# Kernel tuning notes

Hardware: AMD Instinct MI355X
Metric: run time of the kernel (lower is better)

The kernel has to match this reference:

```python
import jax, jax.numpy as jnp
import numpy as np

B, S, D_MODEL, H = 4, 2048, 1024, 16
DEPTH = D_MODEL // H  # 64


def setup_inputs() -> dict:
    key = jax.random.key(0)
    ks = jax.random.split(key, 12)
    inp = {
        "v": jax.random.normal(ks[0], (B, S, D_MODEL), jnp.float32),
        "k": jax.random.normal(ks[1], (B, S, D_MODEL), jnp.float32),
        "q": jax.random.normal(ks[2], (B, S, D_MODEL), jnp.float32),
        "mask": jnp.zeros((B, 1, 1, S), jnp.int32),  # unused by the layer
        # Dense(d_model) params (glorot-ish scale)
        "wq": jax.random.normal(ks[3], (D_MODEL, D_MODEL), jnp.float32) / np.sqrt(D_MODEL),
        "bq": jnp.zeros((D_MODEL,), jnp.float32),
        "wk": jax.random.normal(ks[4], (D_MODEL, D_MODEL), jnp.float32) / np.sqrt(D_MODEL),
        "bk": jnp.zeros((D_MODEL,), jnp.float32),
        "wv": jax.random.normal(ks[5], (D_MODEL, D_MODEL), jnp.float32) / np.sqrt(D_MODEL),
        "bv": jnp.zeros((D_MODEL,), jnp.float32),
        # global attention weights: [max_seq_len, 1], stddev=0.1
        "gqw": 0.1 * jax.random.normal(ks[6], (S, 1), jnp.float32),
        "gkw": 0.1 * jax.random.normal(ks[7], (S, 1), jnp.float32),
        "wo": jax.random.normal(ks[8], (D_MODEL, D_MODEL), jnp.float32) / np.sqrt(D_MODEL),
        "bo": jnp.zeros((D_MODEL,), jnp.float32),
    }
    return inp


def _split_heads(x):
    # [B, S, D] -> [B, H, S, depth]
    Bc = x.shape[0]
    return x.reshape(Bc, -1, H, DEPTH).transpose(0, 2, 1, 3)


def reference(v, k, q, mask, wq, bq, wk, bk, wv, bv, gqw, gkw, wo, bo):
    # QKV projections
    qh = _split_heads(q @ wq + bq)  # [B, H, S, depth]
    kh = _split_heads(k @ wk + bk)
    vh = _split_heads(v @ wv + bv)
    # Fastformer additive attention: mul -> seq-sum -> mul -> seq-sum -> mul -> add
    qh = qh * gqw                          # gqw [S,1] broadcasts over [B,H,S,depth]
    gq = jnp.sum(qh, axis=2, keepdims=True)  # global query [B,H,1,depth]
    kh = kh * gq * gkw
    gk = jnp.sum(kh, axis=2, keepdims=True)  # global key [B,H,1,depth]
    out = vh * gk + qh                       # [B,H,S,depth]
    # merge heads and output projection
    out = out.transpose(0, 2, 1, 3).reshape(out.shape[0], -1, D_MODEL)
    return out @ wo + bo
```

## Files before the change

### kernel.cpp

```cpp
#include <hip/hip_runtime.h>

#define DM 1024
#define BATCH 4
#define SEQ 2048
#define M_TOT (BATCH*SEQ)

typedef unsigned short ushort_t;
typedef __bf16 bf16x8 __attribute__((ext_vector_type(8)));
typedef float f32x4 __attribute__((ext_vector_type(4)));
typedef unsigned short u16x4 __attribute__((ext_vector_type(4)));
typedef unsigned short u16x8 __attribute__((ext_vector_type(8)));

__device__ __forceinline__ ushort_t f2bf(float f) {
  unsigned u = __builtin_bit_cast(unsigned, f);
  u = (u + 0x7fffu + ((u >> 16) & 1u)) >> 16;
  return (ushort_t)u;
}
__device__ __forceinline__ float bf2f(ushort_t h) {
  unsigned u = ((unsigned)h) << 16;
  return __builtin_bit_cast(float, u);
}

#define GLL(gp, lp)                                                            \
  __builtin_amdgcn_global_load_lds(                                            \
      (const __attribute__((address_space(1))) unsigned int*)(const void*)(gp),\
      (__attribute__((address_space(3))) unsigned int*)(void*)(lp), 16, 0, 0)

__global__ void k_reduce(const float* __restrict__ q, const float* __restrict__ k,
                         const float* __restrict__ v,
                         const float* __restrict__ gqw, const float* __restrict__ gkw,
                         float* __restrict__ pq, float* __restrict__ pk,
                         float* __restrict__ G,
                         ushort_t* __restrict__ qb, ushort_t* __restrict__ vb) {
  const int b = blockIdx.x, sc = blockIdx.y;
  const int d0 = threadIdx.x * 4;
  const int s0 = sc * 16;
  const size_t base = ((size_t)b * SEQ + s0) * DM + d0;
  float aq0 = 0.f, aq1 = 0.f, aq2 = 0.f, aq3 = 0.f;
  float ak0 = 0.f, ak1 = 0.f, ak2 = 0.f, ak3 = 0.f;
  float sgq = 0.f, sgk = 0.f;
#pragma unroll 4
  for (int i = 0; i < 16; ++i) {
    const float wq_ = gqw[s0 + i], wk_ = gkw[s0 + i];
    const size_t off = base + (size_t)i * DM;
    const float4 qv = *(const float4*)(q + off);
    const float4 kv = *(const float4*)(k + off);
    const float4 vv = *(const float4*)(v + off);
    aq0 += wq_ * qv.x; aq1 += wq_ * qv.y; aq2 += wq_ * qv.z; aq3 += wq_ * qv.w;
    ak0 += wk_ * kv.x; ak1 += wk_ * kv.y; ak2 += wk_ * kv.z; ak3 += wk_ * kv.w;
    u16x4 oq, ov;
    oq[0] = f2bf(wq_ * qv.x); oq[1] = f2bf(wq_ * qv.y);
    oq[2] = f2bf(wq_ * qv.z); oq[3] = f2bf(wq_ * qv.w);
    ov[0] = f2bf(vv.x); ov[1] = f2bf(vv.y); ov[2] = f2bf(vv.z); ov[3] = f2bf(vv.w);
    *(u16x4*)(qb + off) = oq;
    *(u16x4*)(vb + off) = ov;
    sgq += wq_; sgk += wk_;
  }
  const size_t po = ((size_t)(sc * BATCH + b) << 10) + d0;
  *(float4*)(pq + po) = make_float4(aq0, aq1, aq2, aq3);
  *(float4*)(pk + po) = make_float4(ak0, ak1, ak2, ak3);
  if (b == 0 && threadIdx.x == 0) {
    atomicAdd(&G[0], sgq);
    atomicAdd(&G[1], sgk);
  }
}

__global__ void k_gpart(const float* __restrict__ wq, const float* __restrict__ wk,
                        const float* __restrict__ pq, const float* __restrict__ pk,
                        float* __restrict__ qacc, float* __restrict__ kacc) {
  const int d = blockIdx.x * 256 + threadIdx.x;
  const int k0 = blockIdx.y * 32;
  __shared__ float sq[4][32], sk[4][32];
  if (threadIdx.x < 128) {
    const int b = threadIdx.x >> 5, kk = threadIdx.x & 31;
    float aq = 0.f, ak = 0.f;
#pragma unroll 4
    for (int s = 0; s < 128; ++s) {
      const size_t po = ((size_t)(s * BATCH + b) << 10) + k0 + kk;
      aq += pq[po];
      ak += pk[po];
    }
    sq[b][kk] = aq;
    sk[b][kk] = ak;
  }
  __syncthreads();
  float aq[4] = {0.f, 0.f, 0.f, 0.f}, ak[4] = {0.f, 0.f, 0.f, 0.f};
#pragma unroll 8
  for (int kk = 0; kk < 32; ++kk) {
    const float wqv = wq[(size_t)(k0 + kk) * DM + d];
    const float wkv = wk[(size_t)(k0 + kk) * DM + d];
#pragma unroll
    for (int b = 0; b < 4; ++b) {
      aq[b] += sq[b][kk] * wqv;
      ak[b] += sk[b][kk] * wkv;
    }
  }
#pragma unroll
  for (int b = 0; b < 4; ++b) {
    atomicAdd(&qacc[b * DM + d], aq[b]);
    atomicAdd(&kacc[b * DM + d], ak[b]);
  }
}

__global__ void k_wprep(const float* __restrict__ wq, const float* __restrict__ wv,
                        const float* __restrict__ wo,
                        ushort_t* __restrict__ wqB, ushort_t* __restrict__ wvB,
                        ushort_t* __restrict__ woT) {
  const int bid = blockIdx.x;
  if (bid < 1024) {
    const float* x = bid < 512 ? wq : wv;
    ushort_t* y = bid < 512 ? wqB : wvB;
    size_t i = (size_t)(bid & 511) * 256 + threadIdx.x;
    const float4* p = (const float4*)x + i * 2;
    float4 a = p[0], bb = p[1];
    u16x8 o;
    o[0] = f2bf(a.x); o[1] = f2bf(a.y); o[2] = f2bf(a.z); o[3] = f2bf(a.w);
    o[4] = f2bf(bb.x); o[5] = f2bf(bb.y); o[6] = f2bf(bb.z); o[7] = f2bf(bb.w);
    *(u16x8*)(y + i * 8) = o;
  } else {
    __shared__ float ls[32][33];
    const int t = bid - 1024;
    const int bi = t >> 5, bj = t & 31;
#pragma unroll
    for (int p = 0; p < 4; ++p) {
      int e = threadIdx.x + p * 256;
      int r = e >> 5, c = e & 31;
      ls[r][c] = wo[(size_t)(bi * 32 + r) * DM + bj * 32 + c];
    }
    __syncthreads();
#pragma unroll
    for (int p = 0; p < 4; ++p) {
      int e = threadIdx.x + p * 256;
      int r = e >> 5, c = e & 31;
      woT[(size_t)(bj * 32 + r) * DM + bi * 32 + c] = f2bf(ls[c][r]);
    }
  }
}

__global__ void k_wogbias(const ushort_t* __restrict__ woT, const float* __restrict__ wo,
                          const float* __restrict__ qacc, const float* __restrict__ kacc,
                          const float* __restrict__ bq, const float* __restrict__ bk,
                          const float* __restrict__ bv, const float* __restrict__ G,
                          ushort_t* __restrict__ wogT,
                          float* __restrict__ qbias, float* __restrict__ vbias) {
  const int bid = blockIdx.x;
  const float G0 = G[0], G1 = G[1];
  if (bid < 2048) {
    const size_t i = (size_t)bid * 256 + threadIdx.x;
    const size_t c = i * 8;
    const int j0 = (int)(c & (DM - 1));
    const int b = (int)(c >> 20);
    u16x8 wv8 = *(const u16x8*)(woT + (c & ((1u << 20) - 1)));
    const float4 qa0 = *(const float4*)(qacc + b * DM + j0);
    const float4 qa1 = *(const float4*)(qacc + b * DM + j0 + 4);
    const float4 ka0 = *(const float4*)(kacc + b * DM + j0);
    const float4 ka1 = *(const float4*)(kacc + b * DM + j0 + 4);
    const float4 bq0 = *(const float4*)(bq + j0);
    const float4 bq1 = *(const float4*)(bq + j0 + 4);
    const float4 bk0 = *(const float4*)(bk + j0);
    const float4 bk1 = *(const float4*)(bk + j0 + 4);
    float qa[8] = {qa0.x, qa0.y, qa0.z, qa0.w, qa1.x, qa1.y, qa1.z, qa1.w};
    float ka[8] = {ka0.x, ka0.y, ka0.z, ka0.w, ka1.x, ka1.y, ka1.z, ka1.w};
    float bqv[8] = {bq0.x, bq0.y, bq0.z, bq0.w, bq1.x, bq1.y, bq1.z, bq1.w};
    float bkv[8] = {bk0.x, bk0.y, bk0.z, bk0.w, bk1.x, bk1.y, bk1.z, bk1.w};
    u16x8 o;
#pragma unroll
    for (int j = 0; j < 8; ++j) {
      const float gk = (qa[j] + bqv[j] * G0) * (ka[j] + bkv[j] * G1);
      o[j] = f2bf(bf2f(wv8[j]) * gk);
    }
    *(u16x8*)(wogT + i * 8) = o;
  } else {
    const int t = bid - 2048;
    const int n = (t & 3) * 256 + threadIdx.x;
    const int k0 = (t >> 2) * 32;
    float aq = 0.f, av[4] = {0.f, 0.f, 0.f, 0.f};
    for (int kk = 0; kk < 32; ++kk) {
      const int j = k0 + kk;
      const float w = wo[(size_t)j * DM + n];
      aq += bq[j] * w;
      const float bw = bv[j] * w;
      const float bqj = bq[j] * G0, bkj = bk[j] * G1;
#pragma unroll
      for (int b = 0; b < 4; ++b) {
        const float gkv = (qacc[b * DM + j] + bqj) * (kacc[b * DM + j] + bkj);
        av[b] += bw * gkv;
      }
    }
    atomicAdd(&qbias[n], aq);
#pragma unroll
    for (int b = 0; b < 4; ++b) atomicAdd(&vbias[b * DM + n], av[b]);
  }
}

template <int MODE, int NT>
__global__ __launch_bounds__(512, 1)
void k_pipe(const ushort_t* __restrict__ A0, const ushort_t* __restrict__ B0,
            const ushort_t* __restrict__ A1, const ushort_t* __restrict__ B1,
            const float* __restrict__ gqw, const float* __restrict__ qbias,
            const float* __restrict__ vbias, const float* __restrict__ bo,
            void* __restrict__ OutV) {
  __shared__ __align__(16) ushort_t lsA[3][256 * 64];
  __shared__ __align__(16) ushort_t lsB[3][128 * 64];
  const int tid = threadIdx.x;
  const int w = tid >> 6, lane = tid & 63;
  const int m0 = blockIdx.x * 256, n0 = blockIdx.y * 128;
  const int b = (MODE == 0) ? (m0 >> 11) : 0;
  const int wr = w >> 1, wc = w & 1;

  const ushort_t *Aq, *Bq, *Av = nullptr, *Bv = nullptr;
  if constexpr (MODE == 0) {
    Aq = A0; Bq = B0; Av = A1; Bv = B1 + (size_t)b * (DM * DM);
  } else {
    const int z = blockIdx.z;
    Aq = z ? A1 + (size_t)(z - 1) * (DM * DM) : A0;
    Bq = z ? B1 : B0;
  }

  const int subrow = lane >> 3;
  const int srcslot = (lane & 7) ^ subrow;
  size_t offA[4], offB[2];
#pragma unroll
  for (int p = 0; p < 4; ++p) {
    const int row = (4 * w + p) * 8 + subrow;
    offA[p] = (size_t)(m0 + row) * DM + srcslot * 8;
  }
#pragma unroll
  for (int p = 0; p < 2; ++p) {
    const int row = (2 * w + p) * 8 + subrow;
    offB[p] = (size_t)(n0 + row) * DM + srcslot * 8;
  }

  const int g = lane >> 4, l7 = lane & 7, l15 = lane & 15;
  int aoff[2][4], boff[2][4];
#pragma unroll
  for (int kh = 0; kh < 2; ++kh) {
#pragma unroll
    for (int i = 0; i < 4; ++i) {
      const int ra = wr * 64 + i * 16 + l15;
      aoff[kh][i] = ra * 64 + (((kh * 4 + g) ^ l7) * 8);
    }
#pragma unroll
    for (int j = 0; j < 4; ++j) {
      const int rb = wc * 64 + j * 16 + l15;
      boff[kh][j] = rb * 64 + (((kh * 4 + g) ^ l7) * 8);
    }
  }

  f32x4 acc[4][4];
#pragma unroll
  for (int i = 0; i < 4; ++i)
#pragma unroll
    for (int j = 0; j < 4; ++j) acc[i][j] = (f32x4){0.f, 0.f, 0.f, 0.f};

  auto SRC = [&](int tt, const ushort_t*& Ab, const ushort_t*& Bb, int& k0) {
    if (MODE == 0 && tt >= NT / 2) { Ab = Av; Bb = Bv; k0 = (tt - NT / 2) * 64; }
    else                           { Ab = Aq; Bb = Bq; k0 = tt * 64; }
  };
  auto STAGE_H0 = [&](int tt, int buf) {
    const ushort_t *Ab, *Bb; int k0; SRC(tt, Ab, Bb, k0);
    GLL(Ab + offA[0] + k0, &lsA[buf][(4 * w + 0) * 512]);
    GLL(Ab + offA[1] + k0, &lsA[buf][(4 * w + 1) * 512]);
    GLL(Bb + offB[0] + k0, &lsB[buf][(2 * w + 0) * 512]);
  };
  auto STAGE_H1 = [&](int tt, int buf) {
    const ushort_t *Ab, *Bb; int k0; SRC(tt, Ab, Bb, k0);
    GLL(Ab + offA[2] + k0, &lsA[buf][(4 * w + 2) * 512]);
    GLL(Ab + offA[3] + k0, &lsA[buf][(4 * w + 3) * 512]);
    GLL(Bb + offB[1] + k0, &lsB[buf][(2 * w + 1) * 512]);
  };
  auto READF = [&](bf16x8 (&av)[4], bf16x8 (&bv)[4], int cur, int kh) {
#pragma unroll
    for (int i = 0; i < 4; ++i) av[i] = *(const bf16x8*)(&lsA[cur][aoff[kh][i]]);
#pragma unroll
    for (int j = 0; j < 4; ++j) bv[j] = *(const bf16x8*)(&lsB[cur][boff[kh][j]]);
  };
  auto DOMFMA = [&](bf16x8 (&av)[4], bf16x8 (&bv)[4]) {
    __builtin_amdgcn_s_setprio(1);
#pragma unroll
    for (int i = 0; i < 4; ++i)
#pragma unroll
      for (int j = 0; j < 4; ++j)
        acc[i][j] = __builtin_amdgcn_mfma_f32_16x16x32_bf16(av[i], bv[j], acc[i][j], 0, 0, 0);
    __builtin_amdgcn_s_setprio(0);
  };

  bf16x8 avA[4], bvA[4], avB[4], bvB[4];

  STAGE_H0(0, 0); STAGE_H1(0, 0);
  STAGE_H0(1, 1); STAGE_H1(1, 1);
  asm volatile("s_waitcnt vmcnt(6)" ::: "memory");
  __builtin_amdgcn_s_barrier();
  READF(avA, bvA, 0, 0);

#pragma unroll 1
  for (int t = 0; t < NT; ++t) {
    const int cur = t % 3, nb = (t + 2) % 3, nxt = (t + 1) % 3;
    READF(avB, bvB, cur, 1);
    if (t + 2 < NT) STAGE_H0(t + 2, nb);
    DOMFMA(avA, bvA);
    if (t + 1 < NT) {
      if (t + 2 < NT) { asm volatile("s_waitcnt vmcnt(3)\n\ts_barrier" ::: "memory"); }
      else            { asm volatile("s_waitcnt vmcnt(0)\n\ts_barrier" ::: "memory"); }
      READF(avA, bvA, nxt, 0);
      if (t + 2 < NT) STAGE_H1(t + 2, nb);
    }
    DOMFMA(avB, bvB);
  }

  const int lr = (lane >> 4) * 4, lc = lane & 15;
  const int rbase = m0 + wr * 64, cbase = n0 + wc * 64;
  if constexpr (MODE == 0) {
    float* Out = (float*)OutV;
#pragma unroll
    for (int j = 0; j < 4; ++j) {
      const int col = cbase + j * 16 + lc;
      const float qbn = qbias[col];
      const float cb = vbias[b * DM + col] + bo[col];
#pragma unroll
      for (int i = 0; i < 4; ++i)
#pragma unroll
        for (int r = 0; r < 4; ++r) {
          const int row = rbase + i * 16 + lr + r;
          Out[(size_t)row * DM + col] = acc[i][j][r] + gqw[row & (SEQ - 1)] * qbn + cb;
        }
    }
  } else {
    ushort_t* Out = (ushort_t*)OutV + (size_t)blockIdx.z * (DM * DM);
#pragma unroll
    for (int j = 0; j < 4; ++j) {
      const int col = cbase + j * 16 + lc;
#pragma unroll
      for (int i = 0; i < 4; ++i)
#pragma unroll
        for (int r = 0; r < 4; ++r) {
          const int row = rbase + i * 16 + lr + r;
          Out[(size_t)row * DM + col] = f2bf(acc[i][j][r]);
        }
    }
  }
}

extern "C" void kernel_launch(void* const* d_in, const int* in_sizes, int n_in,
                              void* d_out, int out_size, void* d_ws, size_t ws_size,
                              hipStream_t stream) {
  const float* v   = (const float*)d_in[0];
  const float* k   = (const float*)d_in[1];
  const float* q   = (const float*)d_in[2];
  const float* wq  = (const float*)d_in[4];
  const float* bq  = (const float*)d_in[5];
  const float* wk  = (const float*)d_in[6];
  const float* bk  = (const float*)d_in[7];
  const float* wv  = (const float*)d_in[8];
  const float* bv  = (const float*)d_in[9];
  const float* gqw = (const float*)d_in[10];
  const float* gkw = (const float*)d_in[11];
  const float* wo  = (const float*)d_in[12];
  const float* bo  = (const float*)d_in[13];
  float* out = (float*)d_out;
  float* wsf = (float*)d_ws;

  float* qacc  = wsf + 8192;
  float* kacc  = wsf + 12288;
  float* G     = wsf + 16384;
  float* qbias = wsf + 16640;
  float* vbias = wsf + 17664;
  ushort_t* b16  = (ushort_t*)((char*)d_ws + (1 << 17));
  ushort_t* qb   = b16;
  ushort_t* vb   = qb + (size_t)M_TOT * DM;
  ushort_t* wqB  = vb + (size_t)M_TOT * DM;
  ushort_t* wvB  = wqB + (size_t)DM * DM;
  ushort_t* woT  = wvB + (size_t)DM * DM;
  ushort_t* WqoT = woT + (size_t)DM * DM;
  ushort_t* WvbT = WqoT + (size_t)DM * DM;
  ushort_t* wogT = (ushort_t*)out;
  float* pq = out + (1 << 22);
  float* pk = pq + (1 << 20);

  hipMemsetAsync((char*)d_ws + 8192 * sizeof(float), 0,
                 (21760 - 8192) * sizeof(float), stream);

  k_wprep<<<2048, 256, 0, stream>>>(wq, wv, wo, wqB, wvB, woT);

  k_reduce<<<dim3(BATCH, SEQ / 16), 256, 0, stream>>>(q, k, v, gqw, gkw, pq, pk, G, qb, vb);

  k_gpart<<<dim3(DM / 256, DM / 32), 256, 0, stream>>>(wq, wk, pq, pk, qacc, kacc);

  k_wogbias<<<2176, 256, 0, stream>>>(woT, wo, qacc, kacc, bq, bk, bv, G,
                                      wogT, qbias, vbias);

  k_pipe<1, 16><<<dim3(4, 8, 5), 512, 0, stream>>>(
      woT, wqB, wogT, wvB, nullptr, nullptr, nullptr, nullptr, WqoT);

  k_pipe<0, 32><<<dim3(M_TOT / 256, DM / 128), 512, 0, stream>>>(
      qb, WqoT, vb, WvbT, gqw, qbias, vbias, bo, out);
}
```

Measured before the change: 124.8 us.

## Fuse weight prep into reduce kernel and split partial-sum reduction out of gpart

```diff
diff --git a/kernel.cpp b/kernel.cpp
--- a/kernel.cpp
+++ b/kernel.cpp
@@ -26,91 +26,53 @@
       (const __attribute__((address_space(1))) unsigned int*)(const void*)(gp),\
       (__attribute__((address_space(3))) unsigned int*)(void*)(lp), 16, 0, 0)
 
-__global__ void k_reduce(const float* __restrict__ q, const float* __restrict__ k,
-                         const float* __restrict__ v,
-                         const float* __restrict__ gqw, const float* __restrict__ gkw,
-                         float* __restrict__ pq, float* __restrict__ pk,
-                         float* __restrict__ G,
-                         ushort_t* __restrict__ qb, ushort_t* __restrict__ vb) {
-  const int b = blockIdx.x, sc = blockIdx.y;
-  const int d0 = threadIdx.x * 4;
-  const int s0 = sc * 16;
-  const size_t base = ((size_t)b * SEQ + s0) * DM + d0;
-  float aq0 = 0.f, aq1 = 0.f, aq2 = 0.f, aq3 = 0.f;
-  float ak0 = 0.f, ak1 = 0.f, ak2 = 0.f, ak3 = 0.f;
-  float sgq = 0.f, sgk = 0.f;
+__global__ void k_prep_reduce(const float* __restrict__ q, const float* __restrict__ k,
+                              const float* __restrict__ v,
+                              const float* __restrict__ gqw, const float* __restrict__ gkw,
+                              const float* __restrict__ wq, const float* __restrict__ wv,
+                              const float* __restrict__ wo,
+                              float* __restrict__ pq, float* __restrict__ pk,
+                              float* __restrict__ G,
+                              ushort_t* __restrict__ qb, ushort_t* __restrict__ vb,
+                              ushort_t* __restrict__ wqB, ushort_t* __restrict__ wvB,
+                              ushort_t* __restrict__ woT) {
+  const int bid = blockIdx.x;
+  if (bid < 512) {
+    const int b = bid & 3, sc = bid >> 2;
+    const int d0 = threadIdx.x * 4;
+    const int s0 = sc * 16;
+    const size_t base = ((size_t)b * SEQ + s0) * DM + d0;
+    float aq0 = 0.f, aq1 = 0.f, aq2 = 0.f, aq3 = 0.f;
+    float ak0 = 0.f, ak1 = 0.f, ak2 = 0.f, ak3 = 0.f;
+    float sgq = 0.f, sgk = 0.f;
 #pragma unroll 4
-  for (int i = 0; i < 16; ++i) {
-    const float wq_ = gqw[s0 + i], wk_ = gkw[s0 + i];
-    const size_t off = base + (size_t)i * DM;
-    const float4 qv = *(const float4*)(q + off);
-    const float4 kv = *(const float4*)(k + off);
-    const float4 vv = *(const float4*)(v + off);
-    aq0 += wq_ * qv.x; aq1 += wq_ * qv.y; aq2 += wq_ * qv.z; aq3 += wq_ * qv.w;
-    ak0 += wk_ * kv.x; ak1 += wk_ * kv.y; ak2 += wk_ * kv.z; ak3 += wk_ * kv.w;
-    u16x4 oq, ov;
-    oq[0] = f2bf(wq_ * qv.x); oq[1] = f2bf(wq_ * qv.y);
-    oq[2] = f2bf(wq_ * qv.z); oq[3] = f2bf(wq_ * qv.w);
-    ov[0] = f2bf(vv.x); ov[1] = f2bf(vv.y); ov[2] = f2bf(vv.z); ov[3] = f2bf(vv.w);
-    *(u16x4*)(qb + off) = oq;
-    *(u16x4*)(vb + off) = ov;
-    sgq += wq_; sgk += wk_;
-  }
-  const size_t po = ((size_t)(sc * BATCH + b) << 10) + d0;
-  *(float4*)(pq + po) = make_float4(aq0, aq1, aq2, aq3);
-  *(float4*)(pk + po) = make_float4(ak0, ak1, ak2, ak3);
-  if (b == 0 && threadIdx.x == 0) {
-    atomicAdd(&G[0], sgq);
-    atomicAdd(&G[1], sgk);
-  }
-}
-
-__global__ void k_gpart(const float* __restrict__ wq, const float* __restrict__ wk,
-                        const float* __restrict__ pq, const float* __restrict__ pk,
-                        float* __restrict__ qacc, float* __restrict__ kacc) {
-  const int d = blockIdx.x * 256 + threadIdx.x;
-  const int k0 = blockIdx.y * 32;
-  __shared__ float sq[4][32], sk[4][32];
-  if (threadIdx.x < 128) {
-    const int b = threadIdx.x >> 5, kk = threadIdx.x & 31;
-    float aq = 0.f, ak = 0.f;
-#pragma unroll 4
-    for (int s = 0; s < 128; ++s) {
-      const size_t po = ((size_t)(s * BATCH + b) << 10) + k0 + kk;
-      aq += pq[po];
-      ak += pk[po];
-    }
-    sq[b][kk] = aq;
-    sk[b][kk] = ak;
-  }
-  __syncthreads();
-  float aq[4] = {0.f, 0.f, 0.f, 0.f}, ak[4] = {0.f, 0.f, 0.f, 0.f};
-#pragma unroll 8
-  for (int kk = 0; kk < 32; ++kk) {
-    const float wqv = wq[(size_t)(k0 + kk) * DM + d];
-    const float wkv = wk[(size_t)(k0 + kk) * DM + d];
-#pragma unroll
-    for (int b = 0; b < 4; ++b) {
-      aq[b] += sq[b][kk] * wqv;
-      ak[b] += sk[b][kk] * wkv;
-    }
-  }
-#pragma unroll
-  for (int b = 0; b < 4; ++b) {
-    atomicAdd(&qacc[b * DM + d], aq[b]);
-    atomicAdd(&kacc[b * DM + d], ak[b]);
-  }
-}
-
-__global__ void k_wprep(const float* __restrict__ wq, const float* __restrict__ wv,
-                        const float* __restrict__ wo,
-                        ushort_t* __restrict__ wqB, ushort_t* __restrict__ wvB,
-                        ushort_t* __restrict__ woT) {
-  const int bid = blockIdx.x;
-  if (bid < 1024) {
-    const float* x = bid < 512 ? wq : wv;
-    ushort_t* y = bid < 512 ? wqB : wvB;
-    size_t i = (size_t)(bid & 511) * 256 + threadIdx.x;
+    for (int i = 0; i < 16; ++i) {
+      const float wq_ = gqw[s0 + i], wk_ = gkw[s0 + i];
+      const size_t off = base + (size_t)i * DM;
+      const float4 qv = *(const float4*)(q + off);
+      const float4 kv = *(const float4*)(k + off);
+      const float4 vv = *(const float4*)(v + off);
+      aq0 += wq_ * qv.x; aq1 += wq_ * qv.y; aq2 += wq_ * qv.z; aq3 += wq_ * qv.w;
+      ak0 += wk_ * kv.x; ak1 += wk_ * kv.y; ak2 += wk_ * kv.z; ak3 += wk_ * kv.w;
+      u16x4 oq, ov;
+      oq[0] = f2bf(wq_ * qv.x); oq[1] = f2bf(wq_ * qv.y);
+      oq[2] = f2bf(wq_ * qv.z); oq[3] = f2bf(wq_ * qv.w);
+      ov[0] = f2bf(vv.x); ov[1] = f2bf(vv.y); ov[2] = f2bf(vv.z); ov[3] = f2bf(vv.w);
+      *(u16x4*)(qb + off) = oq;
+      *(u16x4*)(vb + off) = ov;
+      sgq += wq_; sgk += wk_;
+    }
+    const size_t po = ((size_t)(sc * BATCH + b) << 10) + d0;
+    *(float4*)(pq + po) = make_float4(aq0, aq1, aq2, aq3);
+    *(float4*)(pk + po) = make_float4(ak0, ak1, ak2, ak3);
+    if (b == 0 && threadIdx.x == 0) {
+      atomicAdd(&G[0], sgq);
+      atomicAdd(&G[1], sgk);
+    }
+  } else if (bid < 1536) {
+    const float* x = bid < 1024 ? wq : wv;
+    ushort_t* y = bid < 1024 ? wqB : wvB;
+    size_t i = (size_t)((bid - 512) & 511) * 256 + threadIdx.x;
     const float4* p = (const float4*)x + i * 2;
     float4 a = p[0], bb = p[1];
     u16x8 o;
@@ -119,7 +81,7 @@
     *(u16x8*)(y + i * 8) = o;
   } else {
     __shared__ float ls[32][33];
-    const int t = bid - 1024;
+    const int t = bid - 1536;
     const int bi = t >> 5, bj = t & 31;
 #pragma unroll
     for (int p = 0; p < 4; ++p) {
@@ -134,6 +96,52 @@
       int r = e >> 5, c = e & 31;
       woT[(size_t)(bj * 32 + r) * DM + bi * 32 + c] = f2bf(ls[c][r]);
     }
+  }
+}
+
+__global__ void k_rsum(const float* __restrict__ pq, const float* __restrict__ pk,
+                       float* __restrict__ qr, float* __restrict__ kr) {
+  const int b = blockIdx.x;
+  const int d = blockIdx.y * 256 + threadIdx.x;
+  const int sg = blockIdx.z;
+  float aq = 0.f, ak = 0.f;
+#pragma unroll 4
+  for (int s = sg * 32; s < sg * 32 + 32; ++s) {
+    const size_t po = ((size_t)(s * BATCH + b) << 10) + d;
+    aq += pq[po];
+    ak += pk[po];
+  }
+  atomicAdd(&qr[b * DM + d], aq);
+  atomicAdd(&kr[b * DM + d], ak);
+}
+
+__global__ void k_gpart(const float* __restrict__ wq, const float* __restrict__ wk,
+                        const float* __restrict__ qr, const float* __restrict__ kr,
+                        float* __restrict__ qacc, float* __restrict__ kacc) {
+  const int d = blockIdx.x * 256 + threadIdx.x;
+  const int k0 = blockIdx.y * 32;
+  __shared__ float sq[4][32], sk[4][32];
+  if (threadIdx.x < 128) {
+    const int b = threadIdx.x >> 5, kk = threadIdx.x & 31;
+    sq[b][kk] = qr[b * DM + k0 + kk];
+    sk[b][kk] = kr[b * DM + k0 + kk];
+  }
+  __syncthreads();
+  float aq[4] = {0.f, 0.f, 0.f, 0.f}, ak[4] = {0.f, 0.f, 0.f, 0.f};
+#pragma unroll 8
+  for (int kk = 0; kk < 32; ++kk) {
+    const float wqv = wq[(size_t)(k0 + kk) * DM + d];
+    const float wkv = wk[(size_t)(k0 + kk) * DM + d];
+#pragma unroll
+    for (int b = 0; b < 4; ++b) {
+      aq[b] += sq[b][kk] * wqv;
+      ak[b] += sk[b][kk] * wkv;
+    }
+  }
+#pragma unroll
+  for (int b = 0; b < 4; ++b) {
+    atomicAdd(&qacc[b * DM + d], aq[b]);
+    atomicAdd(&kacc[b * DM + d], ak[b]);
   }
 }
 
@@ -360,6 +368,8 @@
   float* out = (float*)d_out;
   float* wsf = (float*)d_ws;
 
+  float* qr    = wsf + 0;
+  float* kr    = wsf + 4096;
   float* qacc  = wsf + 8192;
   float* kacc  = wsf + 12288;
   float* G     = wsf + 16384;
@@ -377,14 +387,14 @@
   float* pq = out + (1 << 22);
   float* pk = pq + (1 << 20);
 
-  hipMemsetAsync((char*)d_ws + 8192 * sizeof(float), 0,
-                 (21760 - 8192) * sizeof(float), stream);
-
-  k_wprep<<<2048, 256, 0, stream>>>(wq, wv, wo, wqB, wvB, woT);
-
-  k_reduce<<<dim3(BATCH, SEQ / 16), 256, 0, stream>>>(q, k, v, gqw, gkw, pq, pk, G, qb, vb);
-
-  k_gpart<<<dim3(DM / 256, DM / 32), 256, 0, stream>>>(wq, wk, pq, pk, qacc, kacc);
+  hipMemsetAsync(d_ws, 0, 21760 * sizeof(float), stream);
+
+  k_prep_reduce<<<2560, 256, 0, stream>>>(q, k, v, gqw, gkw, wq, wv, wo,
+                                          pq, pk, G, qb, vb, wqB, wvB, woT);
+
+  k_rsum<<<dim3(BATCH, DM / 256, 4), 256, 0, stream>>>(pq, pk, qr, kr);
+
+  k_gpart<<<dim3(DM / 256, DM / 32), 256, 0, stream>>>(wq, wk, qr, kr, qacc, kacc);
 
   k_wogbias<<<2176, 256, 0, stream>>>(woT, wo, qacc, kacc, bq, bk, bv, G,
                                       wogT, qbias, vbias);
```

New measurement: 116.8 us. -6.4%, faster.
